# Kernel tuning notes

Measured on AMD Instinct MI355X. Metric: run time of the kernel, lower is better.

Reference implementation:

```python
import jax, jax.numpy as jnp
import numpy as np

N, E, IN_CH, HID, HEADS, OUT_CH = 100000, 1600000, 512, 8, 8, 16
NEG_SLOPE = 0.2


def setup_inputs() -> dict:
    key = jax.random.key(0)
    ks = jax.random.split(key, 10)
    x = jax.random.normal(ks[0], (N, IN_CH), dtype=jnp.float32)
    edge_index = jax.random.randint(ks[1], (2, E), 0, N, dtype=jnp.int64)
    def glorot(k, shape):
        fan = shape[0] + shape[-1]
        s = jnp.sqrt(6.0 / fan)
        return jax.random.uniform(k, shape, jnp.float32, -s, s)
    W1 = glorot(ks[2], (IN_CH, HEADS * HID))          # conv1 linear
    att_l1 = glorot(ks[3], (HEADS, HID)) * 0.5
    att_r1 = glorot(ks[4], (HEADS, HID)) * 0.5
    b1 = jnp.zeros((HEADS * HID,), jnp.float32)
    W2 = glorot(ks[5], (HEADS * HID, HEADS * OUT_CH))  # conv2 linear
    att_l2 = glorot(ks[6], (HEADS, OUT_CH)) * 0.5
    att_r2 = glorot(ks[7], (HEADS, OUT_CH)) * 0.5
    b2 = jnp.zeros((OUT_CH,), jnp.float32)
    return {"x": x, "edge_index": edge_index, "W1": W1, "att_l1": att_l1,
            "att_r1": att_r1, "b1": b1, "W2": W2, "att_l2": att_l2,
            "att_r2": att_r2, "b2": b2}


def supergat_mx_layer(x, src, dst, W, att_l, att_r, bias, heads, ch, concat):
    n = x.shape[0]
    h = (x @ W).reshape(n, heads, ch)            # [N, H, C]
    x_j = h[src]                                 # [E, H, C] gathered source feats
    x_i = h[dst]                                 # [E, H, C] gathered dest feats
    logits = jnp.sum(x_i * x_j, axis=-1)         # MX dot-product gate [E, H]
    alpha = jnp.sum(x_j * att_l, axis=-1) + jnp.sum(x_i * att_r, axis=-1)
    alpha = alpha * jax.nn.sigmoid(logits)
    alpha = jax.nn.leaky_relu(alpha, NEG_SLOPE)
    # segment softmax over destination neighborhoods
    amax = jax.ops.segment_max(alpha, dst, num_segments=n)
    alpha = jnp.exp(alpha - amax[dst])
    denom = jax.ops.segment_sum(alpha, dst, num_segments=n)
    alpha = alpha / (denom[dst] + 1e-16)
    out = jax.ops.segment_sum(x_j * alpha[..., None], dst, num_segments=n)  # [N, H, C]
    out = out.reshape(n, heads * ch) if concat else out.mean(axis=1)
    return out + bias


def reference(x, edge_index, W1, att_l1, att_r1, b1, W2, att_l2, att_r2, b2):
    n = x.shape[0]
    loop = jnp.arange(n, dtype=edge_index.dtype)
    src = jnp.concatenate([edge_index[0], loop])  # add self loops (PyG default)
    dst = jnp.concatenate([edge_index[1], loop])
    h = supergat_mx_layer(x, src, dst, W1, att_l1, att_r1, b1, HEADS, HID, True)
    h = jax.nn.elu(h)
    out = supergat_mx_layer(h, src, dst, W2, att_l2, att_r2, b2, HEADS, OUT_CH, False)
    return jax.nn.log_softmax(out, axis=-1)
```

## Files before the change

### kernel.cpp

```cpp
#include <hip/hip_runtime.h>
#include <hip/hip_fp16.h>
#include <math.h>

#define N_NODES 100000
#define N_EDGES 1600000
#define EPRIME  (N_EDGES + N_NODES)
#define NEG_SLOPE 0.2f
#define LOG2E 1.44269504f
#define NBLK 391
#define NSCAN 99
#define SCHUNK 2048
#define NSCAT (8 * ((N_EDGES + SCHUNK - 1) / SCHUNK))

typedef _Float16 f16x8 __attribute__((ext_vector_type(8)));
typedef float f32x4 __attribute__((ext_vector_type(4)));
typedef float f32x8 __attribute__((ext_vector_type(8)));
typedef float f32x16 __attribute__((ext_vector_type(16)));

__device__ __forceinline__ f32x8 unpack8(float4 r) {
    f32x8 o;
    float2 f;
    f = __half22float2(__builtin_bit_cast(__half2, r.x)); o[0] = f.x; o[1] = f.y;
    f = __half22float2(__builtin_bit_cast(__half2, r.y)); o[2] = f.x; o[3] = f.y;
    f = __half22float2(__builtin_bit_cast(__half2, r.z)); o[4] = f.x; o[5] = f.y;
    f = __half22float2(__builtin_bit_cast(__half2, r.w)); o[6] = f.x; o[7] = f.y;
    return o;
}

__global__ __launch_bounds__(256) void prep_k(const unsigned* __restrict__ eiw,
                                              unsigned* __restrict__ flag,
                                              int* __restrict__ counts,
                                              int* __restrict__ dbins,
                                              const float* __restrict__ W1,
                                              _Float16* __restrict__ W1f) {
    int bid = blockIdx.x;
    int n = bid * 256 + threadIdx.x;
    if (n < N_NODES) counts[n] = 1;
    if (bid == 0) dbins[threadIdx.x] = 0;
    if (bid == 1) {
        __shared__ int any;
        if (threadIdx.x == 0) any = 0;
        __syncthreads();
        int nz = 0;
        for (int i = threadIdx.x; i < 1024; i += 256)
            if (eiw[2 * i + 1] != 0u) nz = 1;
        if (nz) atomicOr(&any, 1);
        __syncthreads();
        if (threadIdx.x == 0) flag[0] = any ? 0u : 1u;
    }
    if (bid >= 2 && bid < 130) {
        int idx = (bid - 2) * 256 + threadIdx.x;
        int j    = idx & 7;
        int lane = (idx >> 3) & 63;
        int nt   = (idx >> 9) & 3;
        int ks   = idx >> 11;
        int k = ks * 32 + (lane >> 4) * 8 + j;
        int c = nt * 16 + (lane & 15);
        W1f[idx] = (_Float16)W1[k * 64 + c];
    }
}

__global__ __launch_bounds__(256) void countrank_k(const int* __restrict__ ei,
                                                   const unsigned* __restrict__ flag,
                                                   int* __restrict__ counts,
                                                   int* __restrict__ rank) {
    int e = blockIdx.x * blockDim.x + threadIdx.x;
    if (e >= N_EDGES) return;
    int d = flag[0] ? ei[2 * (N_EDGES + e)] : ei[N_EDGES + e];
    rank[e] = atomicAdd(&counts[d], 1);
}

__global__ __launch_bounds__(256) void histscan1_k(const int* __restrict__ counts,
                                                   int* __restrict__ dbins,
                                                   int* __restrict__ rowptr,
                                                   int* __restrict__ bsums) {
    __shared__ int s[256];
    int t = threadIdx.x;
    int bid = blockIdx.x;
    if (bid < NBLK) {
        s[t] = 0;
        __syncthreads();
        int n = bid * 256 + t;
        if (n < N_NODES) atomicAdd(&s[min(counts[n], 255)], 1);
        __syncthreads();
        int c = s[t];
        if (c) atomicAdd(&dbins[t], c);
    } else {
        int sb = bid - NBLK;
        int base = sb * 1024 + t * 4;
        int v[4];
#pragma unroll
        for (int j = 0; j < 4; ++j)
            v[j] = (base + j < N_NODES) ? counts[base + j] : 0;
        int tsum = v[0] + v[1] + v[2] + v[3];
        s[t] = tsum;
        __syncthreads();
        for (int off = 1; off < 256; off <<= 1) {
            int x = (t >= off) ? s[t - off] : 0;
            __syncthreads();
            s[t] += x;
            __syncthreads();
        }
        if (t == 255) bsums[sb] = s[255];
        int run = s[t] - tsum;
#pragma unroll
        for (int j = 0; j < 4; ++j) {
            if (base + j <= N_NODES) rowptr[base + j] = run;
            run += v[j];
        }
    }
}

__global__ __launch_bounds__(256) void hscan_scan3_k(const int* __restrict__ dbins,
                                                     int* __restrict__ dstart,
                                                     int* __restrict__ dfill,
                                                     int* __restrict__ rowptr,
                                                     const int* __restrict__ bsums,
                                                     int* __restrict__ col) {
    __shared__ int s[256];
    int t = threadIdx.x;
    if (blockIdx.x == 0) {
        int v = dbins[t];
        s[t] = v;
        __syncthreads();
        for (int off = 1; off < 256; off <<= 1) {
            int x = (t >= off) ? s[t - off] : 0;
            __syncthreads();
            s[t] += x;
            __syncthreads();
        }
        dstart[t] = s[t] - v;
        dfill[t] = 0;
    } else {
        int bid = blockIdx.x - 1;
        s[t] = (t < bid) ? bsums[t] : 0;
        __syncthreads();
        for (int off = 128; off > 0; off >>= 1) {
            if (t < off) s[t] += s[t + off];
            __syncthreads();
        }
        int add = s[0];
        int base = bid * 1024 + t * 4;
#pragma unroll
        for (int j = 0; j < 4; ++j) {
            int idx = base + j;
            if (idx <= N_NODES) {
                int rv = rowptr[idx] + add;
                rowptr[idx] = rv;
                if (idx < N_NODES) col[rv] = idx;
            }
        }
        if (bid == 0 && t < 8) col[EPRIME + t] = 0;
    }
}

__global__ __launch_bounds__(256) void hscat_scat2_k(const int* __restrict__ counts,
                                                     const int* __restrict__ dstart,
                                                     int* __restrict__ dfill,
                                                     int* __restrict__ perm,
                                                     const int* __restrict__ ei,
                                                     const unsigned* __restrict__ flag,
                                                     const int* __restrict__ rowptr,
                                                     const int* __restrict__ rank,
                                                     int* __restrict__ col) {
    if (blockIdx.x < NBLK) {
        __shared__ int lh[256];
        __shared__ int lbase[256];
        lh[threadIdx.x] = 0;
        __syncthreads();
        int n = blockIdx.x * 256 + threadIdx.x;
        int b = 0, lrank = 0;
        bool valid = n < N_NODES;
        if (valid) {
            b = min(counts[n], 255);
            lrank = atomicAdd(&lh[b], 1);
        }
        __syncthreads();
        int c = lh[threadIdx.x];
        lbase[threadIdx.x] = c ? atomicAdd(&dfill[threadIdx.x], c) : 0;
        __syncthreads();
        if (valid) perm[dstart[b] + lbase[b] + lrank] = n;
    } else {
        int sb = blockIdx.x - NBLK;
        int xcd = sb & 7;
        int base = (sb >> 3) * SCHUNK;
        int lo = xcd * 12500, hi = lo + 12500;
        int lim = min(base + SCHUNK, N_EDGES);
        bool f = flag[0] != 0;
        for (int i = base + threadIdx.x; i < lim; i += 256) {
            int d = f ? ei[2 * (N_EDGES + i)] : ei[N_EDGES + i];
            if (d >= lo && d < hi) {
                int s = f ? ei[2 * i] : ei[i];
                col[rowptr[d] + rank[i]] = s;
            }
        }
    }
}

__global__ __launch_bounds__(256) void gemm1_k(const float* __restrict__ x,
                                               const _Float16* __restrict__ W1f,
                                               const float* __restrict__ attl,
                                               const float* __restrict__ attr,
                                               __half* __restrict__ h1,
                                               float* __restrict__ ald,
                                               float* __restrict__ ard) {
    int t = threadIdx.x;
    int w = t >> 6, l = t & 63;
    int rw0 = blockIdx.x * 64 + w * 16;
    int arow = rw0 + (l & 15);
    if (arow >= N_NODES) arow = N_NODES - 1;
    int kg = l >> 4;
    const float4* x4 = (const float4*)(x + (size_t)arow * 512);
    const f16x8* w8 = (const f16x8*)W1f;

    f32x4 acc0 = {0.f, 0.f, 0.f, 0.f};
    f32x4 acc1 = {0.f, 0.f, 0.f, 0.f};
    f32x4 acc2 = {0.f, 0.f, 0.f, 0.f};
    f32x4 acc3 = {0.f, 0.f, 0.f, 0.f};

#pragma unroll 4
    for (int ks = 0; ks < 16; ++ks) {
        float4 a0 = x4[ks * 8 + kg * 2];
        float4 a1 = x4[ks * 8 + kg * 2 + 1];
        f16x8 af;
        af[0] = (_Float16)a0.x; af[1] = (_Float16)a0.y;
        af[2] = (_Float16)a0.z; af[3] = (_Float16)a0.w;
        af[4] = (_Float16)a1.x; af[5] = (_Float16)a1.y;
        af[6] = (_Float16)a1.z; af[7] = (_Float16)a1.w;
        f16x8 b0 = w8[(ks * 4 + 0) * 64 + l];
        f16x8 b1 = w8[(ks * 4 + 1) * 64 + l];
        f16x8 b2 = w8[(ks * 4 + 2) * 64 + l];
        f16x8 b3 = w8[(ks * 4 + 3) * 64 + l];
        acc0 = __builtin_amdgcn_mfma_f32_16x16x32_f16(af, b0, acc0, 0, 0, 0);
        acc1 = __builtin_amdgcn_mfma_f32_16x16x32_f16(af, b1, acc1, 0, 0, 0);
        acc2 = __builtin_amdgcn_mfma_f32_16x16x32_f16(af, b2, acc2, 0, 0, 0);
        acc3 = __builtin_amdgcn_mfma_f32_16x16x32_f16(af, b3, acc3, 0, 0, 0);
    }

    int col = l & 15;
    int hi = col >> 3;
    float al0 = attl[col], al1 = attl[16 + col], al2 = attl[32 + col], al3 = attl[48 + col];
    float ar0 = attr[col], ar1 = attr[16 + col], ar2 = attr[32 + col], ar3 = attr[48 + col];

#pragma unroll
    for (int reg = 0; reg < 4; ++reg) {
        int grow = rw0 + (l >> 4) * 4 + reg;
        bool v = grow < N_NODES;
        float c0 = acc0[reg], c1 = acc1[reg], c2 = acc2[reg], c3 = acc3[reg];
        if (v) {
            __half* hp = h1 + (size_t)grow * 64;
            hp[col]      = __float2half_rn(c0);
            hp[16 + col] = __float2half_rn(c1);
            hp[32 + col] = __float2half_rn(c2);
            hp[48 + col] = __float2half_rn(c3);
        }
        float vl0 = c0 * al0, vl1 = c1 * al1, vl2 = c2 * al2, vl3 = c3 * al3;
        float vr0 = c0 * ar0, vr1 = c1 * ar1, vr2 = c2 * ar2, vr3 = c3 * ar3;
        vl0 += __shfl_xor(vl0, 1); vl1 += __shfl_xor(vl1, 1);
        vl2 += __shfl_xor(vl2, 1); vl3 += __shfl_xor(vl3, 1);
        vr0 += __shfl_xor(vr0, 1); vr1 += __shfl_xor(vr1, 1);
        vr2 += __shfl_xor(vr2, 1); vr3 += __shfl_xor(vr3, 1);
        vl0 += __shfl_xor(vl0, 2); vl1 += __shfl_xor(vl1, 2);
        vl2 += __shfl_xor(vl2, 2); vl3 += __shfl_xor(vl3, 2);
        vr0 += __shfl_xor(vr0, 2); vr1 += __shfl_xor(vr1, 2);
        vr2 += __shfl_xor(vr2, 2); vr3 += __shfl_xor(vr3, 2);
        vl0 += __shfl_xor(vl0, 4); vl1 += __shfl_xor(vl1, 4);
        vl2 += __shfl_xor(vl2, 4); vl3 += __shfl_xor(vl3, 4);
        vr0 += __shfl_xor(vr0, 4); vr1 += __shfl_xor(vr1, 4);
        vr2 += __shfl_xor(vr2, 4); vr3 += __shfl_xor(vr3, 4);
        if (v && (l & 7) == 0) {
            float* alp = ald + (size_t)grow * 8;
            float* arp = ard + (size_t)grow * 8;
            alp[0 + hi] = vl0 * LOG2E; alp[2 + hi] = vl1 * LOG2E;
            alp[4 + hi] = vl2 * LOG2E; alp[6 + hi] = vl3 * LOG2E;
            arp[0 + hi] = vr0 * LOG2E; arp[2 + hi] = vr1 * LOG2E;
            arp[4 + hi] = vr2 * LOG2E; arp[6 + hi] = vr3 * LOG2E;
        }
    }
}

__global__ __launch_bounds__(256) void attn1_k(const __half* __restrict__ h1,
                                               const int* __restrict__ rowptr,
                                               const int* __restrict__ col,
                                               const float* __restrict__ ald,
                                               const float* __restrict__ ard,
                                               const float* __restrict__ b1,
                                               const int* __restrict__ perm,
                                               float* __restrict__ hout) {
    int gid = (blockIdx.x * 256 + threadIdx.x) >> 3;
    int h = threadIdx.x & 7;
    if (gid >= N_NODES) return;
    int node = perm[gid];
    const char* hb = (const char*)h1;
    unsigned hoff = (unsigned)h * 16u;

    f32x8 xi = unpack8(*(const float4*)(hb + (unsigned)node * 128u + hoff));
    float ardi = ard[node * 8 + h];
    int beg = rowptr[node], end = rowptr[node + 1];

    int s0 = col[beg], s1 = col[beg + 1];
    float4 rx0 = *(const float4*)(hb + (unsigned)s0 * 128u + hoff);
    float aj0 = ald[s0 * 8 + h];
    float4 rx1 = *(const float4*)(hb + (unsigned)s1 * 128u + hoff);
    float aj1 = ald[s1 * 8 + h];

    float m2 = -INFINITY, lsum = 0.f;
    f32x8 acc = {0.f, 0.f, 0.f, 0.f, 0.f, 0.f, 0.f, 0.f};
    for (int e = beg; e < end; e += 2) {
        int t0 = col[e + 2], t1 = col[e + 3];
        float4 ry0 = *(const float4*)(hb + (unsigned)t0 * 128u + hoff);
        float c0 = ald[t0 * 8 + h];
        float4 ry1 = *(const float4*)(hb + (unsigned)t1 * 128u + hoff);
        float c1 = ald[t1 * 8 + h];

        f32x8 xj0 = unpack8(rx0);
        f32x8 xj1 = unpack8(rx1);
        float d0 = 0.f, d1 = 0.f;
#pragma unroll
        for (int c = 0; c < 8; ++c) { d0 = fmaf(xi[c], xj0[c], d0); d1 = fmaf(xi[c], xj1[c], d1); }
        float g0 = (aj0 + ardi) * __builtin_amdgcn_rcpf(1.f + __builtin_amdgcn_exp2f(d0 * -LOG2E));
        float g1 = (aj1 + ardi) * __builtin_amdgcn_rcpf(1.f + __builtin_amdgcn_exp2f(d1 * -LOG2E));
        float a0 = fmaxf(g0, NEG_SLOPE * g0);
        float a1 = (e + 1 < end) ? fmaxf(g1, NEG_SLOPE * g1) : -INFINITY;
        float pm = fmaxf(a0, a1);
        if (__any(pm > m2 + 11.5f)) {
            float mn = fmaxf(m2, pm);
            float so = __builtin_amdgcn_exp2f(m2 - mn);
            lsum *= so;
#pragma unroll
            for (int c = 0; c < 8; ++c) acc[c] *= so;
            m2 = mn;
        }
        float p0 = __builtin_amdgcn_exp2f(a0 - m2);
        float p1 = __builtin_amdgcn_exp2f(a1 - m2);
        lsum += p0 + p1;
#pragma unroll
        for (int c = 0; c < 8; ++c) acc[c] += p0 * xj0[c] + p1 * xj1[c];
        rx0 = ry0; aj0 = c0; rx1 = ry1; aj1 = c1;
    }
    float rl = __builtin_amdgcn_rcpf(lsum);
    float4 bv0 = *(const float4*)(b1 + h * 8);
    float4 bv1 = *(const float4*)(b1 + h * 8 + 4);
    float ob[8];
    ob[0] = bv0.x; ob[1] = bv0.y; ob[2] = bv0.z; ob[3] = bv0.w;
    ob[4] = bv1.x; ob[5] = bv1.y; ob[6] = bv1.z; ob[7] = bv1.w;
    float4 o0, o1;
    float* op0 = (float*)&o0;
    float* op1 = (float*)&o1;
#pragma unroll
    for (int c = 0; c < 8; ++c) {
        float o = acc[c] * rl + ob[c];
        o = o > 0.f ? o : (__builtin_amdgcn_exp2f(o * LOG2E) - 1.f);
        if (c < 4) op0[c] = o; else op1[c - 4] = o;
    }
    float4* dst = (float4*)(hout + (size_t)node * 64 + h * 8);
    dst[0] = o0;
    dst[1] = o1;
}

__global__ __launch_bounds__(256) void gemm2_k(const float* __restrict__ h,
                                               const float* __restrict__ W2,
                                               const float* __restrict__ attl,
                                               const float* __restrict__ attr,
                                               __half2* __restrict__ h2,
                                               float* __restrict__ ald,
                                               float* __restrict__ ard) {
    __shared__ float xs[32 * 64];
    int t = threadIdx.x;
    int row0 = blockIdx.x * 32;
    for (int i = t; i < 32 * 16; i += 256) {
        int r = i >> 4, q = i & 15;
        int gr = row0 + r;
        float4 v = make_float4(0.f, 0.f, 0.f, 0.f);
        if (gr < N_NODES) v = ((const float4*)h)[(size_t)gr * 16 + q];
        ((float4*)xs)[r * 16 + q] = v;
    }
    __syncthreads();
    int w = t >> 6, lane = t & 63;
    int r0 = w * 8;
    float2 acc[8];
#pragma unroll
    for (int r = 0; r < 8; ++r) acc[r] = make_float2(0.f, 0.f);
    for (int k = 0; k < 64; ++k) {
        float2 wv = ((const float2*)W2)[k * 64 + lane];
#pragma unroll
        for (int r = 0; r < 8; ++r) {
            float xv = xs[(r0 + r) * 64 + k];
            acc[r].x += xv * wv.x;
            acc[r].y += xv * wv.y;
        }
    }
    float2 al = ((const float2*)attl)[lane];
    float2 ar = ((const float2*)attr)[lane];
#pragma unroll
    for (int r = 0; r < 8; ++r) {
        int gr = row0 + r0 + r;
        float vl = acc[r].x * al.x + acc[r].y * al.y;
        float vr = acc[r].x * ar.x + acc[r].y * ar.y;
        vl += __shfl_xor(vl, 1); vr += __shfl_xor(vr, 1);
        vl += __shfl_xor(vl, 2); vr += __shfl_xor(vr, 2);
        vl += __shfl_xor(vl, 4); vr += __shfl_xor(vr, 4);
        if (gr < N_NODES) {
            h2[(size_t)gr * 64 + lane] = __floats2half2_rn(acc[r].x, acc[r].y);
            if ((lane & 7) == 0) {
                ald[gr * 8 + (lane >> 3)] = vl * LOG2E;
                ard[gr * 8 + (lane >> 3)] = vr * LOG2E;
            }
        }
    }
}

__global__ __launch_bounds__(256) void attn2_k(const __half* __restrict__ h2,
                                               const int* __restrict__ rowptr,
                                               const int* __restrict__ col,
                                               const float* __restrict__ ald,
                                               const float* __restrict__ ard,
                                               const float* __restrict__ b2,
                                               const int* __restrict__ perm,
                                               float* __restrict__ out) {
    int gid = (blockIdx.x * 256 + threadIdx.x) >> 3;
    int h = threadIdx.x & 7;
    if (gid >= N_NODES) return;
    int node = perm[gid];
    const char* hb = (const char*)h2;
    unsigned hoff = (unsigned)h * 32u;

    float4 ri0 = *(const float4*)(hb + (unsigned)node * 256u + hoff);
    float4 ri1 = *(const float4*)(hb + (unsigned)node * 256u + hoff + 16u);
    f32x8 xiA = unpack8(ri0);
    f32x8 xiB = unpack8(ri1);
    float ardi = ard[node * 8 + h];
    int beg = rowptr[node], end = rowptr[node + 1];

    int s0 = col[beg], s1 = col[beg + 1];
    float4 rx0a = *(const float4*)(hb + (unsigned)s0 * 256u + hoff);
    float4 rx0b = *(const float4*)(hb + (unsigned)s0 * 256u + hoff + 16u);
    float aj0 = ald[s0 * 8 + h];
    float4 rx1a = *(const float4*)(hb + (unsigned)s1 * 256u + hoff);
    float4 rx1b = *(const float4*)(hb + (unsigned)s1 * 256u + hoff + 16u);
    float aj1 = ald[s1 * 8 + h];

    float m2 = -INFINITY, lsum = 0.f;
    f32x16 acc;
#pragma unroll
    for (int c = 0; c < 16; ++c) acc[c] = 0.f;

    for (int e = beg; e < end; e += 2) {
        int t0 = col[e + 2], t1 = col[e + 3];
        float4 ry0a = *(const float4*)(hb + (unsigned)t0 * 256u + hoff);
        float4 ry0b = *(const float4*)(hb + (unsigned)t0 * 256u + hoff + 16u);
        float c0 = ald[t0 * 8 + h];
        float4 ry1a = *(const float4*)(hb + (unsigned)t1 * 256u + hoff);
        float4 ry1b = *(const float4*)(hb + (unsigned)t1 * 256u + hoff + 16u);
        float c1 = ald[t1 * 8 + h];

        f32x8 xj0a = unpack8(rx0a), xj0b = unpack8(rx0b);
        f32x8 xj1a = unpack8(rx1a), xj1b = unpack8(rx1b);
        float d0 = 0.f, d1 = 0.f;
#pragma unroll
        for (int c = 0; c < 8; ++c) {
            d0 = fmaf(xiA[c], xj0a[c], d0); d1 = fmaf(xiA[c], xj1a[c], d1);
            d0 = fmaf(xiB[c], xj0b[c], d0); d1 = fmaf(xiB[c], xj1b[c], d1);
        }
        float g0 = (aj0 + ardi) * __builtin_amdgcn_rcpf(1.f + __builtin_amdgcn_exp2f(d0 * -LOG2E));
        float g1 = (aj1 + ardi) * __builtin_amdgcn_rcpf(1.f + __builtin_amdgcn_exp2f(d1 * -LOG2E));
        float a0 = fmaxf(g0, NEG_SLOPE * g0);
        float a1 = (e + 1 < end) ? fmaxf(g1, NEG_SLOPE * g1) : -INFINITY;
        float pm = fmaxf(a0, a1);
        if (__any(pm > m2 + 11.5f)) {
            float mn = fmaxf(m2, pm);
            float so = __builtin_amdgcn_exp2f(m2 - mn);
            lsum *= so;
#pragma unroll
            for (int c = 0; c < 16; ++c) acc[c] *= so;
            m2 = mn;
        }
        float p0 = __builtin_amdgcn_exp2f(a0 - m2);
        float p1 = __builtin_amdgcn_exp2f(a1 - m2);
        lsum += p0 + p1;
#pragma unroll
        for (int c = 0; c < 8; ++c) {
            acc[c]     += p0 * xj0a[c] + p1 * xj1a[c];
            acc[c + 8] += p0 * xj0b[c] + p1 * xj1b[c];
        }
        rx0a = ry0a; rx0b = ry0b; aj0 = c0;
        rx1a = ry1a; rx1b = ry1b; aj1 = c1;
    }

    float rl = __builtin_amdgcn_rcpf(lsum);
    f32x16 v;
#pragma unroll
    for (int c = 0; c < 16; ++c) v[c] = acc[c] * rl;
#pragma unroll
    for (int c = 0; c < 16; ++c) {
        v[c] += __shfl_xor(v[c], 1);
        v[c] += __shfl_xor(v[c], 2);
        v[c] += __shfl_xor(v[c], 4);
    }
    float mx = -INFINITY;
#pragma unroll
    for (int c = 0; c < 16; ++c) { v[c] = v[c] * 0.125f + b2[c]; mx = fmaxf(mx, v[c]); }
    float se = 0.f;
#pragma unroll
    for (int c = 0; c < 16; ++c) se += __expf(v[c] - mx);
    float ls = __logf(se);
    if (h == 0) {
        float4 o;
        float* op = (float*)&o;
        float* dst = out + (size_t)node * 16;
#pragma unroll
        for (int q = 0; q < 4; ++q) {
#pragma unroll
            for (int c = 0; c < 4; ++c) op[c] = v[q * 4 + c] - mx - ls;
            ((float4*)dst)[q] = o;
        }
    }
}

extern "C" void kernel_launch(void* const* d_in, const int* in_sizes, int n_in,
                              void* d_out, int out_size, void* d_ws, size_t ws_size,
                              hipStream_t stream) {
    const float* x     = (const float*)d_in[0];
    const int*   ei    = (const int*)d_in[1];
    const float* W1    = (const float*)d_in[2];
    const float* attl1 = (const float*)d_in[3];
    const float* attr1 = (const float*)d_in[4];
    const float* b1    = (const float*)d_in[5];
    const float* W2    = (const float*)d_in[6];
    const float* attl2 = (const float*)d_in[7];
    const float* attr2 = (const float*)d_in[8];
    const float* b2    = (const float*)d_in[9];
    float* out = (float*)d_out;

    char* ws = (char*)d_ws;
    size_t off = 0;
    auto alloc = [&](size_t bytes) {
        size_t o = off;
        off += (bytes + 255) & ~(size_t)255;
        return o;
    };
    size_t o_flag   = alloc(4);
    size_t o_counts = alloc((size_t)N_NODES * 4);
    size_t o_rank   = alloc((size_t)N_EDGES * 4);
    size_t o_rowptr = alloc((size_t)(N_NODES + 1) * 4);
    size_t o_bsums  = alloc(1024 * 4);
    size_t o_col    = alloc((size_t)(EPRIME + 8) * 4);
    size_t o_h1     = alloc((size_t)N_NODES * 64 * 4);
    size_t o_hout   = alloc((size_t)N_NODES * 64 * 4);
    size_t o_h2     = alloc((size_t)N_NODES * 128 * 4);
    size_t o_w1f    = alloc((size_t)512 * 64 * 2);
    size_t o_perm   = alloc((size_t)N_NODES * 4);
    size_t o_dbins  = alloc(256 * 4);
    size_t o_dstart = alloc(256 * 4);
    size_t o_dfill  = alloc(256 * 4);

    size_t aldsz = ((size_t)N_NODES * 8 * 4 + 255) & ~(size_t)255;
    size_t o_ald1 = o_h2;
    size_t o_ard1 = o_h2 + aldsz;
    size_t o_ald2 = o_h1;
    size_t o_ard2 = o_h1 + aldsz;

    unsigned* flag = (unsigned*)(ws + o_flag);
    int* counts = (int*)(ws + o_counts);
    int* rank   = (int*)(ws + o_rank);
    int* rowptr = (int*)(ws + o_rowptr);
    int* bsums  = (int*)(ws + o_bsums);
    int* col    = (int*)(ws + o_col);
    __half* h1  = (__half*)(ws + o_h1);
    float* hout = (float*)(ws + o_hout);
    __half* h2  = (__half*)(ws + o_h2);
    _Float16* w1f = (_Float16*)(ws + o_w1f);
    int* perm   = (int*)(ws + o_perm);
    int* dbins  = (int*)(ws + o_dbins);
    int* dstart = (int*)(ws + o_dstart);
    int* dfill  = (int*)(ws + o_dfill);
    float* ald1 = (float*)(ws + o_ald1);
    float* ard1 = (float*)(ws + o_ard1);
    float* ald2 = (float*)(ws + o_ald2);
    float* ard2 = (float*)(ws + o_ard2);

    hipLaunchKernelGGL(prep_k, dim3(NBLK), dim3(256), 0, stream,
                       (const unsigned*)ei, flag, counts, dbins, W1, w1f);
    hipLaunchKernelGGL(countrank_k, dim3((N_EDGES + 255) / 256), dim3(256), 0, stream,
                       ei, flag, counts, rank);
    hipLaunchKernelGGL(histscan1_k, dim3(NBLK + NSCAN), dim3(256), 0, stream,
                       counts, dbins, rowptr, bsums);
    hipLaunchKernelGGL(hscan_scan3_k, dim3(1 + NSCAN), dim3(256), 0, stream,
                       dbins, dstart, dfill, rowptr, bsums, col);
    hipLaunchKernelGGL(hscat_scat2_k, dim3(NBLK + NSCAT), dim3(256), 0, stream,
                       counts, dstart, dfill, perm, ei, flag, rowptr, rank, col);
    hipLaunchKernelGGL(gemm1_k, dim3((N_NODES + 63) / 64), dim3(256), 0, stream,
                       x, w1f, attl1, attr1, h1, ald1, ard1);
    hipLaunchKernelGGL(attn1_k, dim3((N_NODES * 8 + 255) / 256), dim3(256), 0, stream,
                       h1, rowptr, col, ald1, ard1, b1, perm, hout);
    hipLaunchKernelGGL(gemm2_k, dim3((N_NODES + 31) / 32), dim3(256), 0, stream,
                       hout, W2, attl2, attr2, (__half2*)h2, ald2, ard2);
    hipLaunchKernelGGL(attn2_k, dim3((N_NODES * 8 + 255) / 256), dim3(256), 0, stream,
                       h2, rowptr, col, ald2, ard2, b2, perm, out);
}
```

Measured before the change: 381.6 us.

## Replace per-edge rank array with XCD-partitioned counting and atomic fill cursors

The edge-count pass no longer records a per-edge rank. It now partitions destinations by XCD-range chunks, the same way the scatter pass does, so each block's atomics stay local to one range. The scatter pass takes slots through atomicAdd on a per-node fill counter instead of reading the stored rank. This removes the 1.6M-entry rank write and read and aims to localise the atomics, at the cost of each block reading its edge chunk eight times. The order of edges inside each CSR row becomes nondeterministic, which can change floating-point summation order.

```diff
diff --git a/kernel.cpp b/kernel.cpp
--- a/kernel.cpp
+++ b/kernel.cpp
@@ -30,12 +30,16 @@
 __global__ __launch_bounds__(256) void prep_k(const unsigned* __restrict__ eiw,
                                               unsigned* __restrict__ flag,
                                               int* __restrict__ counts,
+                                              int* __restrict__ fill,
                                               int* __restrict__ dbins,
                                               const float* __restrict__ W1,
                                               _Float16* __restrict__ W1f) {
     int bid = blockIdx.x;
     int n = bid * 256 + threadIdx.x;
-    if (n < N_NODES) counts[n] = 1;
+    if (n < N_NODES) {
+        counts[n] = 1;
+        fill[n] = 1;
+    }
     if (bid == 0) dbins[threadIdx.x] = 0;
     if (bid == 1) {
         __shared__ int any;
@@ -60,14 +64,18 @@
     }
 }
 
-__global__ __launch_bounds__(256) void countrank_k(const int* __restrict__ ei,
-                                                   const unsigned* __restrict__ flag,
-                                                   int* __restrict__ counts,
-                                                   int* __restrict__ rank) {
-    int e = blockIdx.x * blockDim.x + threadIdx.x;
-    if (e >= N_EDGES) return;
-    int d = flag[0] ? ei[2 * (N_EDGES + e)] : ei[N_EDGES + e];
-    rank[e] = atomicAdd(&counts[d], 1);
+__global__ __launch_bounds__(256) void count_k(const int* __restrict__ ei,
+                                               const unsigned* __restrict__ flag,
+                                               int* __restrict__ counts) {
+    int xcd = blockIdx.x & 7;
+    int base = (blockIdx.x >> 3) * SCHUNK;
+    int lo = xcd * 12500, hi = lo + 12500;
+    int lim = min(base + SCHUNK, N_EDGES);
+    bool f = flag[0] != 0;
+    for (int i = base + threadIdx.x; i < lim; i += 256) {
+        int d = f ? ei[2 * (N_EDGES + i)] : ei[N_EDGES + i];
+        if (d >= lo && d < hi) atomicAdd(&counts[d], 1);
+    }
 }
 
 __global__ __launch_bounds__(256) void histscan1_k(const int* __restrict__ counts,
@@ -161,7 +169,7 @@
                                                      const int* __restrict__ ei,
                                                      const unsigned* __restrict__ flag,
                                                      const int* __restrict__ rowptr,
-                                                     const int* __restrict__ rank,
+                                                     int* __restrict__ fill,
                                                      int* __restrict__ col) {
     if (blockIdx.x < NBLK) {
         __shared__ int lh[256];
@@ -191,7 +199,7 @@
             int d = f ? ei[2 * (N_EDGES + i)] : ei[N_EDGES + i];
             if (d >= lo && d < hi) {
                 int s = f ? ei[2 * i] : ei[i];
-                col[rowptr[d] + rank[i]] = s;
+                col[rowptr[d] + atomicAdd(&fill[d], 1)] = s;
             }
         }
     }
@@ -541,7 +549,7 @@
     };
     size_t o_flag   = alloc(4);
     size_t o_counts = alloc((size_t)N_NODES * 4);
-    size_t o_rank   = alloc((size_t)N_EDGES * 4);
+    size_t o_fill   = alloc((size_t)N_NODES * 4);
     size_t o_rowptr = alloc((size_t)(N_NODES + 1) * 4);
     size_t o_bsums  = alloc(1024 * 4);
     size_t o_col    = alloc((size_t)(EPRIME + 8) * 4);
@@ -562,7 +570,7 @@
 
     unsigned* flag = (unsigned*)(ws + o_flag);
     int* counts = (int*)(ws + o_counts);
-    int* rank   = (int*)(ws + o_rank);
+    int* fill   = (int*)(ws + o_fill);
     int* rowptr = (int*)(ws + o_rowptr);
     int* bsums  = (int*)(ws + o_bsums);
     int* col    = (int*)(ws + o_col);
@@ -580,15 +588,14 @@
     float* ard2 = (float*)(ws + o_ard2);
 
     hipLaunchKernelGGL(prep_k, dim3(NBLK), dim3(256), 0, stream,
-                       (const unsigned*)ei, flag, counts, dbins, W1, w1f);
-    hipLaunchKernelGGL(countrank_k, dim3((N_EDGES + 255) / 256), dim3(256), 0, stream,
-                       ei, flag, counts, rank);
+                       (const unsigned*)ei, flag, counts, fill, dbins, W1, w1f);
+    hipLaunchKernelGGL(count_k, dim3(NSCAT), dim3(256), 0, stream, ei, flag, counts);
     hipLaunchKernelGGL(histscan1_k, dim3(NBLK + NSCAN), dim3(256), 0, stream,
                        counts, dbins, rowptr, bsums);
     hipLaunchKernelGGL(hscan_scan3_k, dim3(1 + NSCAN), dim3(256), 0, stream,
                        dbins, dstart, dfill, rowptr, bsums, col);
     hipLaunchKernelGGL(hscat_scat2_k, dim3(NBLK + NSCAT), dim3(256), 0, stream,
-                       counts, dstart, dfill, perm, ei, flag, rowptr, rank, col);
+                       counts, dstart, dfill, perm, ei, flag, rowptr, fill, col);
     hipLaunchKernelGGL(gemm1_k, dim3((N_NODES + 63) / 64), dim3(256), 0, stream,
                        x, w1f, attl1, attr1, h1, ald1, ard1);
     hipLaunchKernelGGL(attn1_k, dim3((N_NODES * 8 + 255) / 256), dim3(256), 0, stream,
```

Measured after the change: 422.2 us. +10.6%, slower.
